# Kernel tuning notes

Measured on AMD Instinct MI355X. Metric: run time of the kernel, lower is better.

## Reference

```python
import jax, jax.numpy as jnp
import numpy as np
from itertools import combinations

B = 512
N_FEATURES = 64
BINS = 64
N_EMBED = 32
N_HIDDEN = 128
N_OUTPUT = 1
GAMMA = 1.0
TOTAL = N_FEATURES * BINS  # sum(feature_sizes) = 4096


def setup_inputs() -> dict:
    key = jax.random.key(0)
    ks = jax.random.split(key, 20)
    P = N_FEATURES * (N_FEATURES - 1) // 2  # 2016
    mains = jax.random.randint(ks[0], (B, N_FEATURES), 0, BINS, dtype=jnp.int32)
    pairs = jax.random.randint(ks[1], (B, P, 2), 0, BINS, dtype=jnp.int32)
    emb = jax.random.normal(ks[2], (TOTAL, N_EMBED), dtype=jnp.float32) * 0.05
    s = 0.05
    mw0 = jax.random.normal(ks[3], (N_FEATURES, N_EMBED, N_HIDDEN), jnp.float32) * s
    mw1 = jax.random.normal(ks[4], (N_FEATURES, N_HIDDEN, N_HIDDEN), jnp.float32) * s
    mw2 = jax.random.normal(ks[5], (N_FEATURES, N_HIDDEN, N_OUTPUT), jnp.float32) * s
    mb0 = jax.random.normal(ks[6], (N_FEATURES, N_HIDDEN), jnp.float32) * s
    mb1 = jax.random.normal(ks[7], (N_FEATURES, N_HIDDEN), jnp.float32) * s
    mb2 = jax.random.normal(ks[8], (N_FEATURES, N_OUTPUT), jnp.float32) * s
    z_main = jax.random.uniform(ks[9], (N_FEATURES,), jnp.float32, -GAMMA / 100, GAMMA / 100)
    pw0 = jax.random.normal(ks[10], (P, 2 * N_EMBED, N_HIDDEN), jnp.float32) * s
    pw1 = jax.random.normal(ks[11], (P, N_HIDDEN, N_HIDDEN), jnp.float32) * s
    pw2 = jax.random.normal(ks[12], (P, N_HIDDEN, N_OUTPUT), jnp.float32) * s
    pb0 = jax.random.normal(ks[13], (P, N_HIDDEN), jnp.float32) * s
    pb1 = jax.random.normal(ks[14], (P, N_HIDDEN), jnp.float32) * s
    pb2 = jax.random.normal(ks[15], (P, N_OUTPUT), jnp.float32) * s
    z_pairs = jax.random.uniform(ks[16], (P,), jnp.float32, -GAMMA / 100, GAMMA / 100)
    pairs_list = jnp.asarray(np.array(list(combinations(range(N_FEATURES), 2)), dtype=np.int32))
    feature_offsets = (jnp.arange(N_FEATURES, dtype=jnp.int32) * BINS)
    return dict(mains=mains, pairs=pairs, emb=emb,
                mw0=mw0, mw1=mw1, mw2=mw2, mb0=mb0, mb1=mb1, mb2=mb2, z_main=z_main,
                pw0=pw0, pw1=pw1, pw2=pw2, pb0=pb0, pb1=pb1, pb2=pb2, z_pairs=z_pairs,
                pairs_list=pairs_list, feature_offsets=feature_offsets)


def _smooth_z(z):
    g = GAMMA
    smooth = (-2.0 / g ** 3) * z ** 3 + (3.0 / (2.0 * g)) * z + 0.5
    return jnp.where(z <= -g / 2, 0.0, jnp.where(z >= g / 2, 1.0, smooth))


def _grouped_mlp(h, ws, bs):
    # h: [B, G, d_in]; ws[i]: [G, d_in_i, d_out_i]; relu on all but last layer
    n = len(ws)
    for i, (w, b) in enumerate(zip(ws, bs)):
        h = jnp.einsum('bgk,gkl->bgl', h, w) + b[None]
        if i < n - 1:
            h = jax.nn.relu(h)
    return h


def reference(mains, pairs, emb, mw0, mw1, mw2, mb0, mb1, mb2, z_main,
              pw0, pw1, pw2, pb0, pb1, pb2, z_pairs, pairs_list, feature_offsets):
    # main effects: per-feature embedding gather + per-feature MLP
    main_idx = mains + feature_offsets[None, :]             # [B, F]
    h = emb[main_idx]                                        # [B, F, E]
    h = _grouped_mlp(h, [mw0, mw1, mw2], [mb0, mb1, mb2])    # [B, F, O]
    zm = _smooth_z(z_main)                                   # [F]
    out_main = jnp.einsum('bfo,f->bo', h, zm)                # [B, O]
    # pair effects: gather both feature embeddings, concat, per-pair MLP
    pair_off = feature_offsets[pairs_list]                   # [P, 2]
    pair_idx = pairs + pair_off[None]                        # [B, P, 2]
    e = emb[pair_idx]                                        # [B, P, 2, E]
    Bp, P = e.shape[0], e.shape[1]
    e = e.reshape(Bp, P, 2 * e.shape[-1])                    # [B, P, 2E]
    hp = _grouped_mlp(e, [pw0, pw1, pw2], [pb0, pb1, pb2])   # [B, P, O]
    zp = _smooth_z(z_pairs)                                  # [P]
    out_pairs = jnp.einsum('bpo,p->bo', hp, zp)              # [B, O]
    return out_main + out_pairs
```

## Files before the change

### kernel.cpp

```cpp
#include <hip/hip_runtime.h>


typedef _Float16 f16x8 __attribute__((ext_vector_type(8)));
typedef _Float16 f16x4 __attribute__((ext_vector_type(4)));
typedef float f32x4 __attribute__((ext_vector_type(4)));

constexpr int Bsz = 512;
constexpr int NF  = 64;
constexpr int NE  = 32;
constexpr int NH  = 128;
constexpr int NP  = 2016;
constexpr int NG  = NP + NF;
constexpr int BT  = 64;
constexpr int NT  = Bsz / BT;
constexpr int NSEG = 8, GSEG = NG / NSEG;

constexpr size_t WS_S2 = (size_t)NG * Bsz;
constexpr size_t WS_PT = WS_S2 + (size_t)NSEG * Bsz;

__device__ __forceinline__ float smoothz(float z) {
  float s = fmaf(-2.0f * z * z, z, fmaf(1.5f, z, 0.5f));
  if (z <= -0.5f) s = 0.0f;
  if (z >=  0.5f) s = 1.0f;
  return s;
}

__global__ void transpose_pairs_kernel(const int* __restrict__ pairs,
                                       int* __restrict__ pt) {
  __shared__ int tile[32][33];
  const int bt = blockIdx.x;
  const int qt = blockIdx.y;
  const int t  = threadIdx.x;
  const int tq = t & 7, tb = t >> 3;
  const int brow  = bt * 32 + tb;
  const int qbase = qt * 32 + tq * 4;
#pragma unroll
  for (int j = 0; j < 4; ++j)
    tile[tb][tq * 4 + j] = pairs[brow * (2 * NP) + qbase + j];
  __syncthreads();
  const int ob = t & 7, oq = t >> 3;
  const int qrow = qt * 32 + oq;
#pragma unroll
  for (int j = 0; j < 4; ++j)
    pt[(size_t)qrow * Bsz + bt * 32 + ob * 4 + j] = tile[ob * 4 + j][oq];
}

__device__ __forceinline__ f16x8 load_col_frag(const float* __restrict__ p) {
  f16x8 f;
#pragma unroll
  for (int j = 0; j < 8; ++j) f[j] = (_Float16)p[(size_t)(j * NH)];
  return f;
}

__global__ __launch_bounds__(256, 3) void fused_groups_kernel(
    const int* __restrict__ mains, const int* __restrict__ pt,
    const float* __restrict__ emb,
    const float* __restrict__ mw0, const float* __restrict__ mw1,
    const float* __restrict__ mw2, const float* __restrict__ mb0,
    const float* __restrict__ mb1, const float* __restrict__ mb2,
    const float* __restrict__ z_main,
    const float* __restrict__ pw0, const float* __restrict__ pw1,
    const float* __restrict__ pw2, const float* __restrict__ pb0,
    const float* __restrict__ pb1, const float* __restrict__ pb2,
    const float* __restrict__ z_pairs,
    const int* __restrict__ pairs_list, const int* __restrict__ foff,
    float* __restrict__ ws) {
  __shared__ _Float16 sA[BT * 64];
  __shared__ _Float16 sH[BT * NH];
  __shared__ __align__(16) float sBias[3 * NH];
  __shared__ float sRed[4 * BT];

  const int t    = threadIdx.x;
  const int wave = t >> 6;
  const int lane = t & 63;
  const int l    = lane & 15;
  const int qd   = lane >> 4;
  const int g    = blockIdx.x;
  const bool is_pair = (g < NP);

  const float *W0, *W1, *w2p, *bv0, *bv1;
  float b2s, z;
  int off0 = 0, off1 = 0, fid = 0;
  if (is_pair) {
    W0  = pw0 + (size_t)g * (2 * NE * NH);
    W1  = pw1 + (size_t)g * (NH * NH);
    w2p = pw2 + (size_t)g * NH;
    bv0 = pb0 + (size_t)g * NH;
    bv1 = pb1 + (size_t)g * NH;
    b2s = pb2[g];
    z   = smoothz(z_pairs[g]);
    off0 = foff[pairs_list[2 * g + 0]];
    off1 = foff[pairs_list[2 * g + 1]];
  } else {
    fid = g - NP;
    W0  = mw0 + (size_t)fid * (NE * NH);
    W1  = mw1 + (size_t)fid * (NH * NH);
    w2p = mw2 + (size_t)fid * NH;
    bv0 = mb0 + (size_t)fid * NH;
    bv1 = mb1 + (size_t)fid * NH;
    b2s = mb2[fid];
    z   = smoothz(z_main[fid]);
    off0 = foff[fid];
  }

  const int hq = wave * 32 + l;
  f16x8 w0f[2][2];
  f16x8 w1f[2][4];
#pragma unroll
  for (int mh = 0; mh < 2; ++mh) {
    const float* base0 = W0 + (size_t)(qd * 8) * NH + (hq + mh * 16);
    w0f[mh][0] = load_col_frag(base0);
    if (is_pair) w0f[mh][1] = load_col_frag(base0 + (size_t)32 * NH);
  }
#pragma unroll
  for (int mh = 0; mh < 2; ++mh)
#pragma unroll
    for (int kb = 0; kb < 4; ++kb)
      w1f[mh][kb] =
          load_col_frag(W1 + (size_t)(kb * 32 + qd * 8) * NH + (hq + mh * 16));

  if (t < 96) {
    const int which = t >> 5;
    const int i = (t & 31) * 4;
    const float* src = which == 0 ? bv0 : (which == 1 ? bv1 : w2p);
    *(float4*)&sBias[which * NH + i] = *(const float4*)(src + i);
  }

  const int row = t & 63;
  const int q   = t >> 6;
  const int myoff = is_pair ? ((q >> 1) ? off1 : off0) : off0;
  int binv[NT];
  if (is_pair) {
    const size_t pbase = (size_t)(2 * g + (q >> 1)) * Bsz + row;
#pragma unroll
    for (int i = 0; i < NT; ++i) binv[i] = pt[pbase + i * BT];
  } else {
#pragma unroll
    for (int i = 0; i < NT; ++i) binv[i] = mains[(i * BT + row) * NF + fid];
  }

  float4 er0, er1, er2, er3;
  auto ldemb = [&](int bin) {
    const int idx = bin + myoff;
    const float* er =
        emb + (size_t)idx * NE + (is_pair ? ((q & 1) * 16) : (q * 8));
    er0 = ((const float4*)er)[0];
    er1 = ((const float4*)er)[1];
    if (is_pair) {
      er2 = ((const float4*)er)[2];
      er3 = ((const float4*)er)[3];
    }
  };
  auto stemb = [&]() {
    if (is_pair) {
      f16x8 h0, h1;
      h0[0] = (_Float16)er0.x; h0[1] = (_Float16)er0.y;
      h0[2] = (_Float16)er0.z; h0[3] = (_Float16)er0.w;
      h0[4] = (_Float16)er1.x; h0[5] = (_Float16)er1.y;
      h0[6] = (_Float16)er1.z; h0[7] = (_Float16)er1.w;
      h1[0] = (_Float16)er2.x; h1[1] = (_Float16)er2.y;
      h1[2] = (_Float16)er2.z; h1[3] = (_Float16)er2.w;
      h1[4] = (_Float16)er3.x; h1[5] = (_Float16)er3.y;
      h1[6] = (_Float16)er3.z; h1[7] = (_Float16)er3.w;
      const int blk0 = (2 * q)     ^ (row & 7);
      const int blk1 = (2 * q + 1) ^ (row & 7);
      *(f16x8*)&sA[row * 64 + blk0 * 8] = h0;
      *(f16x8*)&sA[row * 64 + blk1 * 8] = h1;
    } else {
      f16x8 h0;
      h0[0] = (_Float16)er0.x; h0[1] = (_Float16)er0.y;
      h0[2] = (_Float16)er0.z; h0[3] = (_Float16)er0.w;
      h0[4] = (_Float16)er1.x; h0[5] = (_Float16)er1.y;
      h0[6] = (_Float16)er1.z; h0[7] = (_Float16)er1.w;
      const int blk = q ^ (row & 7);
      *(f16x8*)&sA[row * 64 + blk * 8] = h0;
    }
  };

  ldemb(binv[0]);
  stemb();
  __syncthreads();

  const int hq4 = wave * 32 + qd * 4;

#pragma unroll
  for (int tile = 0; tile < NT; ++tile) {
    const int bbase = tile * BT;

    if (tile + 1 < NT) ldemb(binv[tile + 1]);

    f32x4 acc0[2][4];
#pragma unroll
    for (int mh = 0; mh < 2; ++mh) {
      const f32x4 b0q = *(const f32x4*)&sBias[hq4 + mh * 16];
#pragma unroll
      for (int nb = 0; nb < 4; ++nb) acc0[mh][nb] = b0q;
    }
#pragma unroll
    for (int nb = 0; nb < 4; ++nb) {
      const int b  = nb * 16 + l;
      const int rs = b & 7;
      const f16x8 e0 = *(const f16x8*)&sA[b * 64 + ((qd ^ rs) * 8)];
      acc0[0][nb] = __builtin_amdgcn_mfma_f32_16x16x32_f16(w0f[0][0], e0,
                                                           acc0[0][nb], 0, 0, 0);
      acc0[1][nb] = __builtin_amdgcn_mfma_f32_16x16x32_f16(w0f[1][0], e0,
                                                           acc0[1][nb], 0, 0, 0);
      if (is_pair) {
        const f16x8 e1 = *(const f16x8*)&sA[b * 64 + (((4 + qd) ^ rs) * 8)];
        acc0[0][nb] = __builtin_amdgcn_mfma_f32_16x16x32_f16(w0f[0][1], e1,
                                                             acc0[0][nb], 0, 0, 0);
        acc0[1][nb] = __builtin_amdgcn_mfma_f32_16x16x32_f16(w0f[1][1], e1,
                                                             acc0[1][nb], 0, 0, 0);
      }
    }

#pragma unroll
    for (int mh = 0; mh < 2; ++mh) {
      const int hb = hq4 + mh * 16;
#pragma unroll
      for (int nb = 0; nb < 4; ++nb) {
        const int b = nb * 16 + l;
        f16x4 h4;
#pragma unroll
        for (int r = 0; r < 4; ++r)
          h4[r] = (_Float16)fmaxf(acc0[mh][nb][r], 0.0f);
        const int blk = (hb >> 3) ^ (b & 7);
        *(f16x4*)&sH[b * NH + blk * 8 + (hb & 7)] = h4;
      }
    }
    __syncthreads();

    if (tile + 1 < NT) stemb();

    f32x4 acc1[2][4];
#pragma unroll
    for (int mh = 0; mh < 2; ++mh) {
      const f32x4 b1q = *(const f32x4*)&sBias[NH + hq4 + mh * 16];
#pragma unroll
      for (int nb = 0; nb < 4; ++nb) acc1[mh][nb] = b1q;
    }
#pragma unroll
    for (int kb = 0; kb < 4; ++kb) {
#pragma unroll
      for (int nb = 0; nb < 4; ++nb) {
        const int b = nb * 16 + l;
        const f16x8 hf =
            *(const f16x8*)&sH[b * NH + (((kb * 4 + qd) ^ (b & 7)) * 8)];
        acc1[0][nb] = __builtin_amdgcn_mfma_f32_16x16x32_f16(w1f[0][kb], hf,
                                                             acc1[0][nb], 0, 0, 0);
        acc1[1][nb] = __builtin_amdgcn_mfma_f32_16x16x32_f16(w1f[1][kb], hf,
                                                             acc1[1][nb], 0, 0, 0);
      }
    }

    float yp[4] = {0.0f, 0.0f, 0.0f, 0.0f};
#pragma unroll
    for (int mh = 0; mh < 2; ++mh) {
      const f32x4 w2q = *(const f32x4*)&sBias[2 * NH + hq4 + mh * 16];
#pragma unroll
      for (int nb = 0; nb < 4; ++nb)
#pragma unroll
        for (int r = 0; r < 4; ++r)
          yp[nb] = fmaf(fmaxf(acc1[mh][nb][r], 0.0f), w2q[r], yp[nb]);
    }
#pragma unroll
    for (int nb = 0; nb < 4; ++nb) {
      yp[nb] += __shfl_xor(yp[nb], 16, 64);
      yp[nb] += __shfl_xor(yp[nb], 32, 64);
    }
    if (qd == 0) {
#pragma unroll
      for (int nb = 0; nb < 4; ++nb) sRed[wave * BT + nb * 16 + l] = yp[nb];
    }

    __syncthreads();
    if (t < BT) {
      const float s =
          sRed[t] + sRed[BT + t] + sRed[2 * BT + t] + sRed[3 * BT + t];
      ws[(size_t)g * Bsz + bbase + t] = (s + b2s) * z;
    }
  }
}

__global__ void reduce1_kernel(const float* __restrict__ part,
                               float* __restrict__ s2) {
  const int b   = blockIdx.x * 256 + threadIdx.x;
  const int seg = blockIdx.y;
  float s = 0.0f;
#pragma unroll 8
  for (int g = seg * GSEG; g < (seg + 1) * GSEG; ++g)
    s += part[(size_t)g * Bsz + b];
  s2[seg * Bsz + b] = s;
}

__global__ void reduce2_kernel(const float* __restrict__ s2,
                               float* __restrict__ out) {
  const int b = blockIdx.x * 256 + threadIdx.x;
  float s = 0.0f;
#pragma unroll
  for (int k = 0; k < NSEG; ++k) s += s2[k * Bsz + b];
  out[b] = s;
}

extern "C" void kernel_launch(void* const* d_in, const int* in_sizes, int n_in,
                              void* d_out, int out_size, void* d_ws,
                              size_t ws_size, hipStream_t stream) {
  const int*   mains      = (const int*)d_in[0];
  const int*   pairs      = (const int*)d_in[1];
  const float* emb        = (const float*)d_in[2];
  const float* mw0        = (const float*)d_in[3];
  const float* mw1        = (const float*)d_in[4];
  const float* mw2        = (const float*)d_in[5];
  const float* mb0        = (const float*)d_in[6];
  const float* mb1        = (const float*)d_in[7];
  const float* mb2        = (const float*)d_in[8];
  const float* z_main     = (const float*)d_in[9];
  const float* pw0        = (const float*)d_in[10];
  const float* pw1        = (const float*)d_in[11];
  const float* pw2        = (const float*)d_in[12];
  const float* pb0        = (const float*)d_in[13];
  const float* pb1        = (const float*)d_in[14];
  const float* pb2        = (const float*)d_in[15];
  const float* z_pairs    = (const float*)d_in[16];
  const int*   pairs_list = (const int*)d_in[17];
  const int*   foff       = (const int*)d_in[18];
  float* ws   = (float*)d_ws;
  float* out  = (float*)d_out;
  float* part = ws;
  float* s2   = ws + WS_S2;
  int*   pt   = (int*)(ws + WS_PT);

  transpose_pairs_kernel<<<dim3(16, 126), 256, 0, stream>>>(pairs, pt);
  fused_groups_kernel<<<NG, 256, 0, stream>>>(
      mains, pt, emb, mw0, mw1, mw2, mb0, mb1, mb2, z_main, pw0, pw1, pw2,
      pb0, pb1, pb2, z_pairs, pairs_list, foff, part);
  reduce1_kernel<<<dim3(2, NSEG), 256, 0, stream>>>(part, s2);
  reduce2_kernel<<<2, 256, 0, stream>>>(s2, out);
}
```

Measured before the change: 336.5 us.

## Stage weights in LDS and keep hidden activations in registers via 32x32 MFMA

Stages the W0 and W1 weights as fp16 in shared memory and gives each wave its own 32 batch columns per iteration. It uses 32x32x16 MFMA so the layer-0 output can be repacked in registers (cvt_pkrtz plus cross-half shuffles) and fed straight in as the B operand of layer 1. This removes the sH shared-memory round trip, the per-tile block barriers and the sRed reduction. The cost is more LDS per block (about 49KB), which may limit occupancy, and repeated A-fragment reads from LDS in place of register-resident weights.

```diff
diff --git a/kernel.cpp b/kernel.cpp
--- a/kernel.cpp
+++ b/kernel.cpp
@@ -2,8 +2,9 @@
 
 
 typedef _Float16 f16x8 __attribute__((ext_vector_type(8)));
-typedef _Float16 f16x4 __attribute__((ext_vector_type(4)));
+typedef __fp16 fp16x2 __attribute__((ext_vector_type(2)));
 typedef float f32x4 __attribute__((ext_vector_type(4)));
+typedef float f32x16 __attribute__((ext_vector_type(16)));
 
 constexpr int Bsz = 512;
 constexpr int NF  = 64;
@@ -11,8 +12,7 @@
 constexpr int NH  = 128;
 constexpr int NP  = 2016;
 constexpr int NG  = NP + NF;
-constexpr int BT  = 64;
-constexpr int NT  = Bsz / BT;
+constexpr int NITER = 4;
 constexpr int NSEG = 8, GSEG = NG / NSEG;
 
 constexpr size_t WS_S2 = (size_t)NG * Bsz;
@@ -43,13 +43,6 @@
 #pragma unroll
   for (int j = 0; j < 4; ++j)
     pt[(size_t)qrow * Bsz + bt * 32 + ob * 4 + j] = tile[ob * 4 + j][oq];
-}
-
-__device__ __forceinline__ f16x8 load_col_frag(const float* __restrict__ p) {
-  f16x8 f;
-#pragma unroll
-  for (int j = 0; j < 8; ++j) f[j] = (_Float16)p[(size_t)(j * NH)];
-  return f;
 }
 
 __global__ __launch_bounds__(256, 3) void fused_groups_kernel(
@@ -65,16 +58,15 @@
     const float* __restrict__ z_pairs,
     const int* __restrict__ pairs_list, const int* __restrict__ foff,
     float* __restrict__ ws) {
-  __shared__ _Float16 sA[BT * 64];
-  __shared__ _Float16 sH[BT * NH];
+  __shared__ _Float16 sW1[NH * NH];
+  __shared__ _Float16 sW0[NH * 64];
   __shared__ __align__(16) float sBias[3 * NH];
-  __shared__ float sRed[4 * BT];
 
   const int t    = threadIdx.x;
   const int wave = t >> 6;
   const int lane = t & 63;
-  const int l    = lane & 15;
-  const int qd   = lane >> 4;
+  const int r    = lane & 31;
+  const int hd   = lane >> 5;
   const int g    = blockIdx.x;
   const bool is_pair = (g < NP);
 
@@ -103,22 +95,36 @@
     off0 = foff[fid];
   }
 
-  const int hq = wave * 32 + l;
-  f16x8 w0f[2][2];
-  f16x8 w1f[2][4];
-#pragma unroll
-  for (int mh = 0; mh < 2; ++mh) {
-    const float* base0 = W0 + (size_t)(qd * 8) * NH + (hq + mh * 16);
-    w0f[mh][0] = load_col_frag(base0);
-    if (is_pair) w0f[mh][1] = load_col_frag(base0 + (size_t)32 * NH);
-  }
-#pragma unroll
-  for (int mh = 0; mh < 2; ++mh)
-#pragma unroll
-    for (int kb = 0; kb < 4; ++kb)
-      w1f[mh][kb] =
-          load_col_frag(W1 + (size_t)(kb * 32 + qd * 8) * NH + (hq + mh * 16));
-
+#pragma unroll
+  for (int i = 0; i < 8; ++i) {
+    const int f = t + i * 256, h = f & 127, kb = f >> 7;
+    f16x8 v;
+#pragma unroll
+    for (int j = 0; j < 8; ++j)
+      v[j] = (_Float16)W1[(size_t)(kb * 8 + j) * NH + h];
+    *(f16x8*)&sW1[h * NH + ((kb ^ (h & 7)) * 8)] = v;
+  }
+  if (is_pair) {
+#pragma unroll
+    for (int i = 0; i < 4; ++i) {
+      const int f = t + i * 256, h = f & 127, kb = f >> 7;
+      f16x8 v;
+#pragma unroll
+      for (int j = 0; j < 8; ++j)
+        v[j] = (_Float16)W0[(size_t)(kb * 8 + j) * NH + h];
+      *(f16x8*)&sW0[h * 64 + ((kb ^ (h & 7)) * 8)] = v;
+    }
+  } else {
+#pragma unroll
+    for (int i = 0; i < 2; ++i) {
+      const int f = t + i * 256, h = f & 127, kb = f >> 7;
+      f16x8 v;
+#pragma unroll
+      for (int j = 0; j < 8; ++j)
+        v[j] = (_Float16)W0[(size_t)(kb * 8 + j) * NH + h];
+      *(f16x8*)&sW0[h * 64 + ((kb ^ (h & 7)) * 8)] = v;
+    }
+  }
   if (t < 96) {
     const int which = t >> 5;
     const int i = (t & 31) * 4;
@@ -126,158 +132,126 @@
     *(float4*)&sBias[which * NH + i] = *(const float4*)(src + i);
   }
 
-  const int row = t & 63;
-  const int q   = t >> 6;
-  const int myoff = is_pair ? ((q >> 1) ? off1 : off0) : off0;
-  int binv[NT];
-  if (is_pair) {
-    const size_t pbase = (size_t)(2 * g + (q >> 1)) * Bsz + row;
-#pragma unroll
-    for (int i = 0; i < NT; ++i) binv[i] = pt[pbase + i * BT];
-  } else {
-#pragma unroll
-    for (int i = 0; i < NT; ++i) binv[i] = mains[(i * BT + row) * NF + fid];
-  }
-
-  float4 er0, er1, er2, er3;
-  auto ldemb = [&](int bin) {
-    const int idx = bin + myoff;
-    const float* er =
-        emb + (size_t)idx * NE + (is_pair ? ((q & 1) * 16) : (q * 8));
-    er0 = ((const float4*)er)[0];
-    er1 = ((const float4*)er)[1];
+  int idxA[NITER], idxB[NITER];
+#pragma unroll
+  for (int i = 0; i < NITER; ++i) {
+    const int col = i * 128 + wave * 32 + r;
     if (is_pair) {
-      er2 = ((const float4*)er)[2];
-      er3 = ((const float4*)er)[3];
+      idxA[i] = pt[(size_t)(2 * g + 0) * Bsz + col] + off0;
+      idxB[i] = pt[(size_t)(2 * g + 1) * Bsz + col] + off1;
+    } else {
+      idxA[i] = mains[col * NF + fid] + off0;
+    }
+  }
+
+  float4 er[8];
+  auto ldemb = [&](int i) {
+    const float* e0 = emb + (size_t)idxA[i] * NE + hd * 8;
+    er[0] = ((const float4*)e0)[0];
+    er[1] = ((const float4*)e0)[1];
+    er[2] = ((const float4*)(e0 + 16))[0];
+    er[3] = ((const float4*)(e0 + 16))[1];
+    if (is_pair) {
+      const float* e1 = emb + (size_t)idxB[i] * NE + hd * 8;
+      er[4] = ((const float4*)e1)[0];
+      er[5] = ((const float4*)e1)[1];
+      er[6] = ((const float4*)(e1 + 16))[0];
+      er[7] = ((const float4*)(e1 + 16))[1];
     }
   };
-  auto stemb = [&]() {
-    if (is_pair) {
-      f16x8 h0, h1;
-      h0[0] = (_Float16)er0.x; h0[1] = (_Float16)er0.y;
-      h0[2] = (_Float16)er0.z; h0[3] = (_Float16)er0.w;
-      h0[4] = (_Float16)er1.x; h0[5] = (_Float16)er1.y;
-      h0[6] = (_Float16)er1.z; h0[7] = (_Float16)er1.w;
-      h1[0] = (_Float16)er2.x; h1[1] = (_Float16)er2.y;
-      h1[2] = (_Float16)er2.z; h1[3] = (_Float16)er2.w;
-      h1[4] = (_Float16)er3.x; h1[5] = (_Float16)er3.y;
-      h1[6] = (_Float16)er3.z; h1[7] = (_Float16)er3.w;
-      const int blk0 = (2 * q)     ^ (row & 7);
-      const int blk1 = (2 * q + 1) ^ (row & 7);
-      *(f16x8*)&sA[row * 64 + blk0 * 8] = h0;
-      *(f16x8*)&sA[row * 64 + blk1 * 8] = h1;
-    } else {
-      f16x8 h0;
-      h0[0] = (_Float16)er0.x; h0[1] = (_Float16)er0.y;
-      h0[2] = (_Float16)er0.z; h0[3] = (_Float16)er0.w;
-      h0[4] = (_Float16)er1.x; h0[5] = (_Float16)er1.y;
-      h0[6] = (_Float16)er1.z; h0[7] = (_Float16)er1.w;
-      const int blk = q ^ (row & 7);
-      *(f16x8*)&sA[row * 64 + blk * 8] = h0;
-    }
-  };
-
-  ldemb(binv[0]);
-  stemb();
+
+  ldemb(0);
   __syncthreads();
 
-  const int hq4 = wave * 32 + qd * 4;
-
-#pragma unroll
-  for (int tile = 0; tile < NT; ++tile) {
-    const int bbase = tile * BT;
-
-    if (tile + 1 < NT) ldemb(binv[tile + 1]);
-
-    f32x4 acc0[2][4];
-#pragma unroll
-    for (int mh = 0; mh < 2; ++mh) {
-      const f32x4 b0q = *(const f32x4*)&sBias[hq4 + mh * 16];
-#pragma unroll
-      for (int nb = 0; nb < 4; ++nb) acc0[mh][nb] = b0q;
-    }
-#pragma unroll
-    for (int nb = 0; nb < 4; ++nb) {
-      const int b  = nb * 16 + l;
-      const int rs = b & 7;
-      const f16x8 e0 = *(const f16x8*)&sA[b * 64 + ((qd ^ rs) * 8)];
-      acc0[0][nb] = __builtin_amdgcn_mfma_f32_16x16x32_f16(w0f[0][0], e0,
-                                                           acc0[0][nb], 0, 0, 0);
-      acc0[1][nb] = __builtin_amdgcn_mfma_f32_16x16x32_f16(w0f[1][0], e0,
-                                                           acc0[1][nb], 0, 0, 0);
-      if (is_pair) {
-        const f16x8 e1 = *(const f16x8*)&sA[b * 64 + (((4 + qd) ^ rs) * 8)];
-        acc0[0][nb] = __builtin_amdgcn_mfma_f32_16x16x32_f16(w0f[0][1], e1,
-                                                             acc0[0][nb], 0, 0, 0);
-        acc0[1][nb] = __builtin_amdgcn_mfma_f32_16x16x32_f16(w0f[1][1], e1,
-                                                             acc0[1][nb], 0, 0, 0);
-      }
-    }
-
-#pragma unroll
-    for (int mh = 0; mh < 2; ++mh) {
-      const int hb = hq4 + mh * 16;
-#pragma unroll
-      for (int nb = 0; nb < 4; ++nb) {
-        const int b = nb * 16 + l;
-        f16x4 h4;
-#pragma unroll
-        for (int r = 0; r < 4; ++r)
-          h4[r] = (_Float16)fmaxf(acc0[mh][nb][r], 0.0f);
-        const int blk = (hb >> 3) ^ (b & 7);
-        *(f16x4*)&sH[b * NH + blk * 8 + (hb & 7)] = h4;
-      }
-    }
-    __syncthreads();
-
-    if (tile + 1 < NT) stemb();
-
-    f32x4 acc1[2][4];
-#pragma unroll
-    for (int mh = 0; mh < 2; ++mh) {
-      const f32x4 b1q = *(const f32x4*)&sBias[NH + hq4 + mh * 16];
-#pragma unroll
-      for (int nb = 0; nb < 4; ++nb) acc1[mh][nb] = b1q;
-    }
-#pragma unroll
-    for (int kb = 0; kb < 4; ++kb) {
-#pragma unroll
-      for (int nb = 0; nb < 4; ++nb) {
-        const int b = nb * 16 + l;
-        const f16x8 hf =
-            *(const f16x8*)&sH[b * NH + (((kb * 4 + qd) ^ (b & 7)) * 8)];
-        acc1[0][nb] = __builtin_amdgcn_mfma_f32_16x16x32_f16(w1f[0][kb], hf,
-                                                             acc1[0][nb], 0, 0, 0);
-        acc1[1][nb] = __builtin_amdgcn_mfma_f32_16x16x32_f16(w1f[1][kb], hf,
-                                                             acc1[1][nb], 0, 0, 0);
-      }
-    }
-
-    float yp[4] = {0.0f, 0.0f, 0.0f, 0.0f};
-#pragma unroll
-    for (int mh = 0; mh < 2; ++mh) {
-      const f32x4 w2q = *(const f32x4*)&sBias[2 * NH + hq4 + mh * 16];
-#pragma unroll
-      for (int nb = 0; nb < 4; ++nb)
-#pragma unroll
-        for (int r = 0; r < 4; ++r)
-          yp[nb] = fmaf(fmaxf(acc1[mh][nb][r], 0.0f), w2q[r], yp[nb]);
-    }
-#pragma unroll
-    for (int nb = 0; nb < 4; ++nb) {
-      yp[nb] += __shfl_xor(yp[nb], 16, 64);
-      yp[nb] += __shfl_xor(yp[nb], 32, 64);
-    }
-    if (qd == 0) {
-#pragma unroll
-      for (int nb = 0; nb < 4; ++nb) sRed[wave * BT + nb * 16 + l] = yp[nb];
-    }
-
-    __syncthreads();
-    if (t < BT) {
-      const float s =
-          sRed[t] + sRed[BT + t] + sRed[2 * BT + t] + sRed[3 * BT + t];
-      ws[(size_t)g * Bsz + bbase + t] = (s + b2s) * z;
+#pragma unroll
+  for (int iter = 0; iter < NITER; ++iter) {
+    f32x16 acc[4];
+#pragma unroll
+    for (int m = 0; m < 4; ++m)
+#pragma unroll
+      for (int q = 0; q < 4; ++q) {
+        const f32x4 b = *(const f32x4*)&sBias[m * 32 + q * 8 + 4 * hd];
+        acc[m][4 * q + 0] = b[0]; acc[m][4 * q + 1] = b[1];
+        acc[m][4 * q + 2] = b[2]; acc[m][4 * q + 3] = b[3];
+      }
+
+#pragma unroll
+    for (int kc = 0; kc < 4; ++kc) {
+      if (kc < 2 || is_pair) {
+        f16x8 bf;
+        bf[0] = (_Float16)er[2 * kc].x; bf[1] = (_Float16)er[2 * kc].y;
+        bf[2] = (_Float16)er[2 * kc].z; bf[3] = (_Float16)er[2 * kc].w;
+        bf[4] = (_Float16)er[2 * kc + 1].x; bf[5] = (_Float16)er[2 * kc + 1].y;
+        bf[6] = (_Float16)er[2 * kc + 1].z; bf[7] = (_Float16)er[2 * kc + 1].w;
+#pragma unroll
+        for (int m = 0; m < 4; ++m) {
+          const f16x8 a = *(const f16x8*)
+              &sW0[(m * 32 + r) * 64 + (((2 * kc + hd) ^ (r & 7)) * 8)];
+          acc[m] = __builtin_amdgcn_mfma_f32_32x32x16_f16(a, bf, acc[m], 0, 0, 0);
+        }
+      }
+    }
+
+    if (iter + 1 < NITER) ldemb(iter + 1);
+
+    f16x8 hb[8];
+#pragma unroll
+    for (int a2 = 0; a2 < 4; ++a2) {
+      float D[8], Q[8];
+#pragma unroll
+      for (int p = 0; p < 8; ++p) {
+        const float lo = fmaxf(acc[a2][2 * p], 0.0f);
+        const float hi = fmaxf(acc[a2][2 * p + 1], 0.0f);
+        const fp16x2 pk = __builtin_amdgcn_cvt_pkrtz(lo, hi);
+        D[p] = __builtin_bit_cast(float, pk);
+        Q[p] = __shfl_xor(D[p], 32, 64);
+      }
+#pragma unroll
+      for (int b = 0; b < 2; ++b) {
+        f32x4 w;
+        if (hd == 0) {
+          w[0] = D[4 * b + 0]; w[1] = D[4 * b + 1];
+          w[2] = Q[4 * b + 0]; w[3] = Q[4 * b + 1];
+        } else {
+          w[0] = Q[4 * b + 2]; w[1] = Q[4 * b + 3];
+          w[2] = D[4 * b + 2]; w[3] = D[4 * b + 3];
+        }
+        hb[2 * a2 + b] = __builtin_bit_cast(f16x8, w);
+      }
+    }
+
+#pragma unroll
+    for (int m = 0; m < 4; ++m)
+#pragma unroll
+      for (int q = 0; q < 4; ++q) {
+        const f32x4 b = *(const f32x4*)&sBias[NH + m * 32 + q * 8 + 4 * hd];
+        acc[m][4 * q + 0] = b[0]; acc[m][4 * q + 1] = b[1];
+        acc[m][4 * q + 2] = b[2]; acc[m][4 * q + 3] = b[3];
+      }
+
+#pragma unroll
+    for (int kc = 0; kc < 8; ++kc)
+#pragma unroll
+      for (int m = 0; m < 4; ++m) {
+        const f16x8 a = *(const f16x8*)
+            &sW1[(m * 32 + r) * NH + (((2 * kc + hd) ^ (r & 7)) * 8)];
+        acc[m] = __builtin_amdgcn_mfma_f32_32x32x16_f16(a, hb[kc], acc[m], 0, 0, 0);
+      }
+
+    float y = 0.0f;
+#pragma unroll
+    for (int m = 0; m < 4; ++m)
+#pragma unroll
+      for (int q = 0; q < 4; ++q) {
+        const f32x4 w2q = *(const f32x4*)&sBias[2 * NH + m * 32 + q * 8 + 4 * hd];
+#pragma unroll
+        for (int i2 = 0; i2 < 4; ++i2)
+          y = fmaf(fmaxf(acc[m][4 * q + i2], 0.0f), w2q[i2], y);
+      }
+    y += __shfl_xor(y, 32, 64);
+    if (lane < 32) {
+      const int col = iter * 128 + wave * 32 + r;
+      ws[(size_t)g * Bsz + col] = (y + b2s) * z;
     }
   }
 }
```

New measurement: 343.4 us. 2.1% more time.
